# Performance work log

Hardware: AMD Instinct MI355X
Metric: run time of the kernel (lower is better)

## Reference

```python
import jax, jax.numpy as jnp
import numpy as np

EPSILON = 1e-07
ROUGH_K = 50
NEG_SLOPE = 0.01  # LeakyReLU default


def setup_inputs() -> dict:
    key = jax.random.key(0)
    ks = jax.random.split(key, 12)
    n, d = 2048, 512
    demb = 64
    hid = 512
    pair_emb = 3 * d + demb
    s = lambda fan: 1.0 / np.sqrt(fan)
    return {
        "word_features": jax.random.normal(ks[0], (n, d), jnp.float32),
        "W_ih": jax.random.normal(ks[1], (4 * d, d), jnp.float32) * s(d),
        "W_hh": jax.random.normal(ks[2], (4 * d, d), jnp.float32) * s(d),
        "b_ih": jax.random.normal(ks[3], (4 * d,), jnp.float32) * s(d),
        "b_hh": jax.random.normal(ks[4], (4 * d,), jnp.float32) * s(d),
        "bil_W": jax.random.normal(ks[5], (d, d), jnp.float32) * s(d),
        "bil_b": jax.random.normal(ks[6], (d,), jnp.float32) * s(d),
        "dist_emb": jax.random.normal(ks[7], (9, demb), jnp.float32),
        "hid_W": jax.random.normal(ks[8], (hid, pair_emb), jnp.float32) * s(pair_emb),
        "hid_b": jax.random.normal(ks[9], (hid,), jnp.float32) * s(pair_emb),
        "out_W": jax.random.normal(ks[10], (1, hid), jnp.float32) * s(hid),
        "out_b": jax.random.normal(ks[11], (1,), jnp.float32) * s(hid),
    }


def _lstm(x, W_ih, W_hh, b_ih, b_hh):
    # x: [n, d]; single-layer unidirectional LSTM, torch gate order i,f,g,o
    n, d = x.shape
    xp = x @ W_ih.T + (b_ih + b_hh)  # [n, 4d]

    def step(carry, xp_t):
        h, c = carry
        gates = xp_t + h @ W_hh.T
        i, f, g, o = jnp.split(gates, 4)
        i, f, o = jax.nn.sigmoid(i), jax.nn.sigmoid(f), jax.nn.sigmoid(o)
        g = jnp.tanh(g)
        c = f * c + i * g
        h = o * jnp.tanh(c)
        return (h, c), h

    h0 = jnp.zeros((d,), x.dtype)
    (_, _), hs = jax.lax.scan(step, (h0, h0), xp)
    return hs  # [n, d]


def reference(word_features, W_ih, W_hh, b_ih, b_hh, bil_W, bil_b,
              dist_emb, hid_W, hid_b, out_W, out_b):
    words = _lstm(word_features, W_ih, W_hh, b_ih, b_hh)  # [n, d]
    n = words.shape[0]

    # --- RoughScorer: strict lower-triangular mask + bilinear scores ---
    ids = jnp.arange(n)
    pair_mask = jnp.where(ids[:, None] > ids[None, :], 0.0, -jnp.inf)
    bilinear_scores = (words @ bil_W.T + bil_b) @ words.T  # [n, n]
    rough = pair_mask + bilinear_scores
    top_scores, top_idx = jax.lax.top_k(rough, ROUGH_K)  # [n, k]

    # --- DistancePairwiseEncoder ---
    dist = jnp.maximum(ids[:, None] - ids[top_idx], 1)  # [n, k]
    log_d = jnp.minimum(jnp.floor(jnp.log2(dist.astype(jnp.float32))), 6.0).astype(jnp.int32)
    d_idx = jnp.where(dist < 5, dist - 1, log_d + 2)  # in [0, 8]
    pairwise = dist_emb[d_idx]  # [n, k, demb]

    # --- AnaphoricityScorer: gather -> concat -> FFNN ---
    b_mentions = words[top_idx]  # [n, k, d]
    a_mentions = jnp.broadcast_to(words[:, None, :], b_mentions.shape)
    pair = jnp.concatenate(
        (a_mentions, b_mentions, a_mentions * b_mentions, pairwise), axis=2)
    h = pair @ hid_W.T + hid_b  # [n, k, hid]
    h = jnp.where(h >= 0, h, NEG_SLOPE * h)  # LeakyReLU
    fine = (h @ out_W.T + out_b)[..., 0]  # [n, k]
    scores = top_scores + fine
    # add_dummy(eps=True): prepend epsilon column
    dummy = jnp.full((n, 1), EPSILON, scores.dtype)
    coref_scores = jnp.concatenate((dummy, scores), axis=1)  # [n, k+1]
    return coref_scores, top_idx
```

## Files before the change

kernel.cpp:

```cpp
#include <hip/hip_runtime.h>
#include <math.h>

#define N_TOK 2048
#define DIM   512
#define K_TOP 50
#define NWG_LSTM 16

typedef short bf16x8 __attribute__((ext_vector_type(8)));
typedef float f32x4  __attribute__((ext_vector_type(4)));

static __device__ inline unsigned bfr(float x) {
  unsigned u = __float_as_uint(x);
  return (u + 0x7fffu + ((u >> 16) & 1u)) >> 16;
}

__global__ __launch_bounds__(256) void init_kernel(unsigned long long* hbuf) {
  int t = threadIdx.x;
  for (int k = t; k < 1024; k += 256) hbuf[k] = 0ull;
}

__global__ __launch_bounds__(256) void gemm_nt(
    const float* __restrict__ A, int lda,
    const float* __restrict__ B, int ldb,
    float* __restrict__ C, int ldc,
    const float* __restrict__ bias1, const float* __restrict__ bias2,
    int M, int N, int K)
{
  __shared__ float As[16][64];
  __shared__ float Bs[16][64];
  const int tid = threadIdx.x;
  const int bm = blockIdx.y, bn = blockIdx.x;
  const int tx = tid & 15, ty = tid >> 4;
  const int lr = tid >> 2;
  const int lk = (tid & 3) << 2;
  const int arow = bm*64 + lr;
  const int brow = bn*64 + lr;
  float acc[4][4];
  #pragma unroll
  for (int a = 0; a < 4; ++a)
    #pragma unroll
    for (int b = 0; b < 4; ++b) acc[a][b] = 0.0f;

  for (int k0 = 0; k0 < K; k0 += 16) {
    float4 av = make_float4(0.f,0.f,0.f,0.f);
    float4 bv = make_float4(0.f,0.f,0.f,0.f);
    if (arow < M) av = *(const float4*)(A + (size_t)arow*lda + k0 + lk);
    if (brow < N) bv = *(const float4*)(B + (size_t)brow*ldb + k0 + lk);
    __syncthreads();
    As[lk+0][lr]=av.x; As[lk+1][lr]=av.y; As[lk+2][lr]=av.z; As[lk+3][lr]=av.w;
    Bs[lk+0][lr]=bv.x; Bs[lk+1][lr]=bv.y; Bs[lk+2][lr]=bv.z; Bs[lk+3][lr]=bv.w;
    __syncthreads();
    #pragma unroll
    for (int k = 0; k < 16; ++k) {
      float4 a4 = *(const float4*)(&As[k][ty<<2]);
      float4 b4 = *(const float4*)(&Bs[k][tx<<2]);
      float aa[4] = {a4.x,a4.y,a4.z,a4.w};
      float bb[4] = {b4.x,b4.y,b4.z,b4.w};
      #pragma unroll
      for (int ii = 0; ii < 4; ++ii)
        #pragma unroll
        for (int jj = 0; jj < 4; ++jj)
          acc[ii][jj] = fmaf(aa[ii], bb[jj], acc[ii][jj]);
    }
  }
  const int n0 = bn*64 + (tx<<2);
  float bc[4] = {0.f,0.f,0.f,0.f};
  if (bias1) {
    #pragma unroll
    for (int q = 0; q < 4; ++q) bc[q] += bias1[n0+q];
  }
  if (bias2) {
    #pragma unroll
    for (int q = 0; q < 4; ++q) bc[q] += bias2[n0+q];
  }
  #pragma unroll
  for (int ii = 0; ii < 4; ++ii) {
    int m = bm*64 + (ty<<2) + ii;
    if (m < M) {
      float4 o;
      o.x = acc[ii][0]+bc[0]; o.y = acc[ii][1]+bc[1];
      o.z = acc[ii][2]+bc[2]; o.w = acc[ii][3]+bc[3];
      *(float4*)(C + (size_t)m*ldc + n0) = o;
    }
  }
}

__global__ __launch_bounds__(256) void gemm_nt128(
    const float* __restrict__ A, int lda,
    const float* __restrict__ B, int ldb,
    float* __restrict__ C, int ldc,
    const float* __restrict__ bias1, const float* __restrict__ bias2,
    int K)
{
  __shared__ float As[16][128];
  __shared__ float Bs[16][128];
  const int tid = threadIdx.x;
  const int bm = blockIdx.y, bn = blockIdx.x;
  const int tx = tid & 15, ty = tid >> 4;
  const int sr = tid >> 1;
  const int sk = (tid & 1) << 3;

  const float* Ar = A + (size_t)(bm*128 + sr)*lda + sk;
  const float* Br = B + (size_t)(bn*128 + sr)*ldb + sk;

  float acc[8][8];
  #pragma unroll
  for (int r = 0; r < 8; ++r)
    #pragma unroll
    for (int c = 0; c < 8; ++c) acc[r][c] = 0.0f;

  float4 a0r = *(const float4*)(Ar + 0);
  float4 a1r = *(const float4*)(Ar + 4);
  float4 b0r = *(const float4*)(Br + 0);
  float4 b1r = *(const float4*)(Br + 4);
  {
    As[sk+0][sr]=a0r.x; As[sk+1][sr]=a0r.y; As[sk+2][sr]=a0r.z; As[sk+3][sr]=a0r.w;
    As[sk+4][sr]=a1r.x; As[sk+5][sr]=a1r.y; As[sk+6][sr]=a1r.z; As[sk+7][sr]=a1r.w;
    Bs[sk+0][sr]=b0r.x; Bs[sk+1][sr]=b0r.y; Bs[sk+2][sr]=b0r.z; Bs[sk+3][sr]=b0r.w;
    Bs[sk+4][sr]=b1r.x; Bs[sk+5][sr]=b1r.y; Bs[sk+6][sr]=b1r.z; Bs[sk+7][sr]=b1r.w;
  }
  __syncthreads();

  for (int k0 = 0; k0 < K; k0 += 16) {
    const bool more = (k0 + 16) < K;
    if (more) {
      a0r = *(const float4*)(Ar + k0+16);
      a1r = *(const float4*)(Ar + k0+20);
      b0r = *(const float4*)(Br + k0+16);
      b1r = *(const float4*)(Br + k0+20);
    }
    #pragma unroll
    for (int k = 0; k < 16; ++k) {
      float4 a0 = *(const float4*)(&As[k][ty<<3]);
      float4 a1 = *(const float4*)(&As[k][(ty<<3)+4]);
      float4 b0 = *(const float4*)(&Bs[k][tx<<3]);
      float4 b1 = *(const float4*)(&Bs[k][(tx<<3)+4]);
      float aa[8] = {a0.x,a0.y,a0.z,a0.w,a1.x,a1.y,a1.z,a1.w};
      float bb[8] = {b0.x,b0.y,b0.z,b0.w,b1.x,b1.y,b1.z,b1.w};
      #pragma unroll
      for (int r = 0; r < 8; ++r)
        #pragma unroll
        for (int c = 0; c < 8; ++c)
          acc[r][c] = fmaf(aa[r], bb[c], acc[r][c]);
    }
    if (more) {
      __syncthreads();
      As[sk+0][sr]=a0r.x; As[sk+1][sr]=a0r.y; As[sk+2][sr]=a0r.z; As[sk+3][sr]=a0r.w;
      As[sk+4][sr]=a1r.x; As[sk+5][sr]=a1r.y; As[sk+6][sr]=a1r.z; As[sk+7][sr]=a1r.w;
      Bs[sk+0][sr]=b0r.x; Bs[sk+1][sr]=b0r.y; Bs[sk+2][sr]=b0r.z; Bs[sk+3][sr]=b0r.w;
      Bs[sk+4][sr]=b1r.x; Bs[sk+5][sr]=b1r.y; Bs[sk+6][sr]=b1r.z; Bs[sk+7][sr]=b1r.w;
      __syncthreads();
    }
  }

  const int n0 = bn*128 + (tx<<3);
  float bc[8] = {0,0,0,0,0,0,0,0};
  if (bias1) {
    #pragma unroll
    for (int c = 0; c < 8; ++c) bc[c] += bias1[n0+c];
  }
  if (bias2) {
    #pragma unroll
    for (int c = 0; c < 8; ++c) bc[c] += bias2[n0+c];
  }
  #pragma unroll
  for (int r = 0; r < 8; ++r) {
    int m = bm*128 + (ty<<3) + r;
    float4 o0, o1;
    o0.x=acc[r][0]+bc[0]; o0.y=acc[r][1]+bc[1]; o0.z=acc[r][2]+bc[2]; o0.w=acc[r][3]+bc[3];
    o1.x=acc[r][4]+bc[4]; o1.y=acc[r][5]+bc[5]; o1.z=acc[r][6]+bc[6]; o1.w=acc[r][7]+bc[7];
    *(float4*)(C + (size_t)m*ldc + n0)     = o0;
    *(float4*)(C + (size_t)m*ldc + n0 + 4) = o1;
  }
}

__global__ __launch_bounds__(512, 2) void lstm_kernel(
    const float* __restrict__ W_hh,
    const float* __restrict__ xp,
    float* __restrict__ words,
    unsigned long long* __restrict__ hbuf)
{
  if (blockIdx.x & 7) return;
  const int wg  = blockIdx.x >> 3;
  const int tid = threadIdx.x;
  const int row_l = tid >> 2;
  const int q     = tid & 3;
  const int g  = row_l >> 5;
  const int cl = row_l & 31;
  const int cell = (wg<<5) + cl;
  const int grow = (g<<9) + cell;

  float4 wv[32];
  {
    const float4* wp = (const float4*)(W_hh + (size_t)grow*512 + (q<<7));
    #pragma unroll
    for (int k = 0; k < 32; ++k) wv[k] = wp[k];
  }

  __shared__ float h_lds[2][4*132];
  __shared__ float gates_lds[128];
  float c_state = 0.0f;

  for (int t = 0; t < N_TOK; ++t) {
    float xg = xp[(size_t)t*2048 + grow];

    {
      const unsigned long long* src = hbuf + ((t & 1) << 9) + tid;
      unsigned long long v;
      do {
        v = __hip_atomic_load(src, __ATOMIC_RELAXED, __HIP_MEMORY_SCOPE_AGENT);
      } while ((unsigned)(v >> 32) != (unsigned)t);
      h_lds[t & 1][(tid >> 7)*132 + (tid & 127)] = __uint_as_float((unsigned)v);
    }
    __syncthreads();

    const float4* hv4 = (const float4*)(h_lds[t & 1] + q*132);
    float a0=0.f,a1=0.f,a2=0.f,a3=0.f;
    #pragma unroll
    for (int k = 0; k < 32; ++k) {
      float4 hv = hv4[k];
      a0 = fmaf(wv[k].x, hv.x, a0);
      a1 = fmaf(wv[k].y, hv.y, a1);
      a2 = fmaf(wv[k].z, hv.z, a2);
      a3 = fmaf(wv[k].w, hv.w, a3);
    }
    float acc = (a0+a1)+(a2+a3);
    acc += __shfl_xor(acc, 1);
    acc += __shfl_xor(acc, 2);
    if (q == 0) {
      float gate = acc + xg;
      gates_lds[row_l] = (g == 2) ? tanhf(gate) : 1.0f/(1.0f + expf(-gate));
    }
    __syncthreads();
    if (tid < 32) {
      float iv = gates_lds[tid];
      float fv = gates_lds[32+tid];
      float gv = gates_lds[64+tid];
      float ov = gates_lds[96+tid];
      c_state = fmaf(fv, c_state, iv*gv);
      float h = ov * tanhf(c_state);
      unsigned long long pv =
          ((unsigned long long)(unsigned)(t+1) << 32) |
          (unsigned long long)__float_as_uint(h);
      __hip_atomic_store(hbuf + (((t+1) & 1) << 9) + (wg<<5) + tid, pv,
                         __ATOMIC_RELAXED, __HIP_MEMORY_SCOPE_AGENT);
      words[(size_t)t*512 + (wg<<5) + tid] = h;
    }
  }
}

__global__ __launch_bounds__(256) void topk_kernel(
    const float* __restrict__ rough,
    float* __restrict__ tsc,
    int* __restrict__ tidx)
{
  const int i = blockIdx.x;
  const int tid = threadIdx.x;
  float v[8];
  #pragma unroll
  for (int s = 0; s < 8; ++s) {
    int j = (s<<8) + tid;
    v[s] = (j < i) ? rough[(size_t)i*N_TOK + j] : -__builtin_inff();
  }
  __shared__ float rv[4];
  __shared__ int   ri[4];
  __shared__ int   wsh;
  for (int p = 0; p < K_TOP; ++p) {
    if (p >= i) {
      if (tid == 0) { tsc[i*K_TOP+p] = -1.0e30f; tidx[i*K_TOP+p] = p; }
      continue;
    }
    float m = -__builtin_inff(); int mi = 0x7fffffff;
    #pragma unroll
    for (int s = 0; s < 8; ++s) {
      int j = (s<<8) + tid;
      bool b = (v[s] > m);
      m = b ? v[s] : m; mi = b ? j : mi;
    }
    #pragma unroll
    for (int off = 32; off > 0; off >>= 1) {
      float m2 = __shfl_xor(m, off);
      int   i2 = __shfl_xor(mi, off);
      bool b = (m2 > m) || (m2 == m && i2 < mi);
      m = b ? m2 : m; mi = b ? i2 : mi;
    }
    if ((tid & 63) == 0) { rv[tid>>6] = m; ri[tid>>6] = mi; }
    __syncthreads();
    if (tid == 0) {
      #pragma unroll
      for (int wv = 1; wv < 4; ++wv) {
        bool b = (rv[wv] > m) || (rv[wv] == m && ri[wv] < mi);
        m = b ? rv[wv] : m; mi = b ? ri[wv] : mi;
      }
      tsc[i*K_TOP+p] = m;
      tidx[i*K_TOP+p] = mi;
      wsh = mi;
    }
    __syncthreads();
    const int widx = wsh;
    if ((widx & 255) == tid) {
      #pragma unroll
      for (int s = 0; s < 8; ++s) if ((widx >> 8) == s) v[s] = -__builtin_inff();
    }
  }
}

__global__ __launch_bounds__(256) void pack_wc(const float* __restrict__ hid_W,
                                               bf16x8* __restrict__ WcB) {
  int id = blockIdx.x*256 + threadIdx.x;
  int c  = id & 15;
  int lg = (id >> 4) & 3;
  int ks = (id >> 6) & 15;
  int nt = id >> 10;
  const float* src = hid_W + (size_t)(nt*16 + c)*1600 + 1024 + ks*32 + lg*8;
  bf16x8 v;
  #pragma unroll
  for (int e = 0; e < 8; ++e) v[e] = (short)bfr(src[e]);
  WcB[id] = v;
}

__global__ __launch_bounds__(256) void pair_kernel(
    const float* __restrict__ words,
    const bf16x8* __restrict__ WcB,
    const float* __restrict__ Aproj,
    const float* __restrict__ Bproj,
    const float* __restrict__ Eproj,
    const float* __restrict__ outW,
    const float* __restrict__ out_b,
    const float* __restrict__ tsc,
    const int* __restrict__ tidx,
    float* __restrict__ out)
{
  __shared__ unsigned m_lds[64*256];
  __shared__ int   j_sm[K_TOP];
  __shared__ int   d_sm[K_TOP];
  __shared__ float s_sm[K_TOP];
  const int i = blockIdx.x;
  const int tid = threadIdx.x;

  if (tid < K_TOP) {
    int j = tidx[i*K_TOP + tid];
    int dist = i - j; if (dist < 1) dist = 1;
    int didx;
    if (dist < 5) didx = dist - 1;
    else { int l = 31 - __clz(dist); if (l > 6) l = 6; didx = l + 2; }
    j_sm[tid] = j; d_sm[tid] = didx;
    s_sm[tid] = tsc[i*K_TOP + tid];
  }
  __syncthreads();

  {
    const int k4 = tid & 127;
    const int r0 = tid >> 7;
    const int kb = k4 >> 1, half = k4 & 1;
    const float4 a4 = *(const float4*)(words + (size_t)i*DIM + (k4<<2));
    for (int r = r0; r < K_TOP; r += 2) {
      const float4 w4 = *(const float4*)(words + (size_t)j_sm[r]*DIM + (k4<<2));
      unsigned lo = bfr(a4.x*w4.x) | (bfr(a4.y*w4.y) << 16);
      unsigned hi = bfr(a4.z*w4.z) | (bfr(a4.w*w4.w) << 16);
      unsigned off = (unsigned)r*256 + (unsigned)((kb ^ (r&7))<<2) + (half<<1);
      m_lds[off]   = lo;
      m_lds[off+1] = hi;
    }
    for (int r = K_TOP + r0; r < 64; r += 2) {
      unsigned off = (unsigned)r*256 + (unsigned)((kb ^ (r&7))<<2) + (half<<1);
      m_lds[off] = 0u; m_lds[off+1] = 0u;
    }
  }
  __syncthreads();

  const int w    = tid >> 6;
  const int lane = tid & 63;
  const int c    = lane & 15;
  const int lg   = lane >> 4;
  const int row  = (w << 4) + c;

  f32x4 acc[32];
  #pragma unroll
  for (int nt = 0; nt < 32; ++nt) acc[nt] = (f32x4){0.f,0.f,0.f,0.f};

  for (int ks = 0; ks < 16; ++ks) {
    const int kb = (ks << 2) + lg;
    bf16x8 a = *(const bf16x8*)(m_lds + (unsigned)row*256 + (unsigned)((kb ^ (row&7))<<2));
    const bf16x8* wbp = WcB + ((ks << 6) + (lg << 4) + c);
    #pragma unroll
    for (int nt = 0; nt < 32; ++nt) {
      bf16x8 b = wbp[nt << 10];
      acc[nt] = __builtin_amdgcn_mfma_f32_16x16x32_bf16(a, b, acc[nt], 0, 0, 0);
    }
  }

  const float ob = out_b[0];
  const int srow0 = (w << 4) + (lg << 2);
  const float* bpr[4];
  const float* epr[4];
  #pragma unroll
  for (int reg = 0; reg < 4; ++reg) {
    int srow = srow0 + reg;
    int jr = (srow < K_TOP) ? j_sm[srow] : 0;
    int dr = (srow < K_TOP) ? d_sm[srow] : 0;
    bpr[reg] = Bproj + (size_t)jr*DIM;
    epr[reg] = Eproj + (size_t)dr*DIM;
  }
  float p[4] = {0.f,0.f,0.f,0.f};
  #pragma unroll
  for (int nt = 0; nt < 32; ++nt) {
    int col = (nt << 4) + c;
    float ap = Aproj[(size_t)i*DIM + col];
    float ow = outW[col];
    #pragma unroll
    for (int reg = 0; reg < 4; ++reg) {
      float v = acc[nt][reg] + ap + bpr[reg][col] + epr[reg][col];
      v = (v >= 0.f) ? v : 0.01f*v;
      p[reg] = fmaf(v, ow, p[reg]);
    }
  }
  #pragma unroll
  for (int reg = 0; reg < 4; ++reg) {
    #pragma unroll
    for (int off = 1; off < 16; off <<= 1) p[reg] += __shfl_xor(p[reg], off);
  }
  if (c == 0) {
    #pragma unroll
    for (int reg = 0; reg < 4; ++reg) {
      int srow = srow0 + reg;
      if (srow < K_TOP) out[(size_t)i*51 + 1 + srow] = s_sm[srow] + p[reg] + ob;
    }
  }
  if (tid == 0) out[(size_t)i*51] = 1e-7f;
}

extern "C" void kernel_launch(void* const* d_in, const int* in_sizes, int n_in,
                              void* d_out, int out_size, void* d_ws, size_t ws_size,
                              hipStream_t stream) {
  const float* wf       = (const float*)d_in[0];
  const float* W_ih     = (const float*)d_in[1];
  const float* W_hh     = (const float*)d_in[2];
  const float* b_ih     = (const float*)d_in[3];
  const float* b_hh     = (const float*)d_in[4];
  const float* bil_W    = (const float*)d_in[5];
  const float* bil_b    = (const float*)d_in[6];
  const float* dist_emb = (const float*)d_in[7];
  const float* hid_W    = (const float*)d_in[8];
  const float* hid_b    = (const float*)d_in[9];
  const float* out_W    = (const float*)d_in[10];
  const float* out_b    = (const float*)d_in[11];
  (void)in_sizes; (void)n_in; (void)out_size; (void)ws_size;

  float* ws    = (float*)d_ws;
  float* xp    = ws;
  float* rough = ws;
  float* words = ws + 4*1024*1024;
  float* tmp   = words + N_TOK*DIM;
  float* Aproj = tmp   + N_TOK*DIM;
  float* Bproj = Aproj + N_TOK*DIM;
  float* Eproj = Bproj + N_TOK*DIM;
  bf16x8* WcB  = (bf16x8*)(Eproj + 8192);
  float* tsc   = Eproj + 8192 + 131072;
  unsigned long long* hbuf = (unsigned long long*)(tsc + 102400);

  float* out_f  = (float*)d_out;
  int*   idx_out = (int*)(out_f + N_TOK*(K_TOP+1));

  dim3 blk(256);
  init_kernel<<<1, blk, 0, stream>>>(hbuf);
  gemm_nt128<<<dim3(16,16), blk, 0, stream>>>(wf, DIM, W_ih, DIM, xp, 2048,
                                              b_ih, b_hh, DIM);
  lstm_kernel<<<NWG_LSTM*8, 512, 0, stream>>>(W_hh, xp, words, hbuf);
  gemm_nt128<<<dim3(4,16), blk, 0, stream>>>(words, DIM, bil_W, DIM, tmp, DIM,
                                             bil_b, nullptr, DIM);
  gemm_nt128<<<dim3(16,16), blk, 0, stream>>>(tmp, DIM, words, DIM, rough, 2048,
                                              nullptr, nullptr, DIM);
  gemm_nt128<<<dim3(4,16), blk, 0, stream>>>(words, DIM, hid_W,       1600, Aproj, DIM,
                                             hid_b, nullptr, DIM);
  gemm_nt128<<<dim3(4,16), blk, 0, stream>>>(words, DIM, hid_W + 512, 1600, Bproj, DIM,
                                             nullptr, nullptr, DIM);
  gemm_nt<<<dim3(8,1), blk, 0, stream>>>(dist_emb, 64, hid_W + 1536, 1600, Eproj, DIM,
                                         nullptr, nullptr, 9, DIM, 64);
  pack_wc<<<128, blk, 0, stream>>>(hid_W, WcB);
  topk_kernel<<<N_TOK, blk, 0, stream>>>(rough, tsc, idx_out);
  pair_kernel<<<N_TOK, blk, 0, stream>>>(words, WcB, Aproj, Bproj, Eproj,
                                         out_W, out_b, tsc, idx_out, out_f);
}
```

Before: 3.647 ms.

## Remap LSTM threads so gate combine stays in-wavefront, dropping second barrier

Threads are remapped so that the four gate rows (i,f,g,o) of a cell, each split across four lanes, fall in one 64-lane wavefront. The cell update is then done with cross-lane shuffles instead of a shared-memory round trip and a second __syncthreads per timestep. The polling loop for the hidden-state handoff is also changed to keep two atomic loads in flight instead of one. Activation and cell math is now computed redundantly in every lane, and the extra outstanding polling loads add memory traffic.

```diff
diff --git a/kernel.cpp b/kernel.cpp
--- a/kernel.cpp
+++ b/kernel.cpp
@@ -183,12 +183,13 @@
   if (blockIdx.x & 7) return;
   const int wg  = blockIdx.x >> 3;
   const int tid = threadIdx.x;
-  const int row_l = tid >> 2;
-  const int q     = tid & 3;
-  const int g  = row_l >> 5;
-  const int cl = row_l & 31;
-  const int cell = (wg<<5) + cl;
-  const int grow = (g<<9) + cell;
+  const int wvid = tid >> 6;
+  const int lane = tid & 63;
+  const int clw  = lane >> 4;
+  const int g    = (lane >> 2) & 3;
+  const int q    = lane & 3;
+  const int cell = (wg << 5) + (wvid << 2) + clw;
+  const int grow = (g << 9) + cell;
 
   float4 wv[32];
   {
@@ -198,19 +199,25 @@
   }
 
   __shared__ float h_lds[2][4*132];
-  __shared__ float gates_lds[128];
   float c_state = 0.0f;
+  const int wrpos = (tid >> 7)*132 + (tid & 127);
 
   for (int t = 0; t < N_TOK; ++t) {
     float xg = xp[(size_t)t*2048 + grow];
 
     {
       const unsigned long long* src = hbuf + ((t & 1) << 9) + tid;
-      unsigned long long v;
-      do {
-        v = __hip_atomic_load(src, __ATOMIC_RELAXED, __HIP_MEMORY_SCOPE_AGENT);
-      } while ((unsigned)(v >> 32) != (unsigned)t);
-      h_lds[t & 1][(tid >> 7)*132 + (tid & 127)] = __uint_as_float((unsigned)v);
+      unsigned long long v = __hip_atomic_load(src, __ATOMIC_RELAXED, __HIP_MEMORY_SCOPE_AGENT);
+      if ((unsigned)(v >> 32) != (unsigned)t) {
+        unsigned long long v2 = __hip_atomic_load(src, __ATOMIC_RELAXED, __HIP_MEMORY_SCOPE_AGENT);
+        for (;;) {
+          v = __hip_atomic_load(src, __ATOMIC_RELAXED, __HIP_MEMORY_SCOPE_AGENT);
+          if ((unsigned)(v2 >> 32) == (unsigned)t) { v = v2; break; }
+          v2 = __hip_atomic_load(src, __ATOMIC_RELAXED, __HIP_MEMORY_SCOPE_AGENT);
+          if ((unsigned)(v >> 32) == (unsigned)t) break;
+        }
+      }
+      h_lds[t & 1][wrpos] = __uint_as_float((unsigned)v);
     }
     __syncthreads();
 
@@ -227,24 +234,24 @@
     float acc = (a0+a1)+(a2+a3);
     acc += __shfl_xor(acc, 1);
     acc += __shfl_xor(acc, 2);
-    if (q == 0) {
-      float gate = acc + xg;
-      gates_lds[row_l] = (g == 2) ? tanhf(gate) : 1.0f/(1.0f + expf(-gate));
-    }
-    __syncthreads();
-    if (tid < 32) {
-      float iv = gates_lds[tid];
-      float fv = gates_lds[32+tid];
-      float gv = gates_lds[64+tid];
-      float ov = gates_lds[96+tid];
-      c_state = fmaf(fv, c_state, iv*gv);
-      float h = ov * tanhf(c_state);
+    float gate = acc + xg;
+    gate = (g == 2) ? tanhf(gate) : 1.0f/(1.0f + expf(-gate));
+
+    const int base = (lane & 48) | q;
+    float iv = __shfl(gate, base);
+    float fv = __shfl(gate, base + 4);
+    float gv = __shfl(gate, base + 8);
+    float ov = __shfl(gate, base + 12);
+    c_state = fmaf(fv, c_state, iv*gv);
+    float h = ov * tanhf(c_state);
+
+    if ((lane & 15) == 0) {
       unsigned long long pv =
           ((unsigned long long)(unsigned)(t+1) << 32) |
           (unsigned long long)__float_as_uint(h);
-      __hip_atomic_store(hbuf + (((t+1) & 1) << 9) + (wg<<5) + tid, pv,
+      __hip_atomic_store(hbuf + (((t+1) & 1) << 9) + cell, pv,
                          __ATOMIC_RELAXED, __HIP_MEMORY_SCOPE_AGENT);
-      words[(size_t)t*512 + (wg<<5) + tid] = h;
+      words[(size_t)t*512 + cell] = h;
     }
   }
 }
```

Result: slower. 6.721 ms (+84.3%).
